# Kernel optimization log

Measured on AMD Instinct MI355X. Metric: run time of the kernel, lower is better.

## Reference

```python
import jax, jax.numpy as jnp
import numpy as np

NUM_NODES = 40000
NUM_REL = 474
ENT_DIM = 100
REL_DIM = 100
NHID = 100
NHEADS = 2
OUT_DIM = NHID * NHEADS  # 200
ALPHA = 0.2
NUM_ORTHO_HEADS = 2
ORTHO_LAMBDA = 0.01
EPS = 1e-12


def _l2norm(x):
    n = jnp.sqrt(jnp.sum(x * x, axis=1, keepdims=True))
    return x / jnp.maximum(n, EPS)


def _leaky_relu(x):
    return jnp.where(x >= 0, x, ALPHA * x)


def _ortho_loss(a):
    # orthogonality penalty between the NUM_ORTHO_HEADS row-blocks of `a`
    Af = a.reshape(NUM_ORTHO_HEADS, -1)
    Afn = Af / jnp.maximum(jnp.linalg.norm(Af, axis=1, keepdims=True), EPS)
    G = Afn @ Afn.T
    return ORTHO_LAMBDA * jnp.sum((G - jnp.eye(NUM_ORTHO_HEADS, dtype=a.dtype)) ** 2)


def _gat_layer(x, tgt, src, rel, a, a2, concat):
    # x: [N, f]; tgt/src: [E]; rel: [E, r]; a: [out, 2f+r]; a2: [out]
    f = x.shape[1]
    a_t, a_s, a_r = a[:, :f], a[:, f:2 * f], a[:, 2 * f:]
    # edge_m = a @ concat(x[tgt], x[src], rel)^T, computed without materializing the concat
    edge_m = x[tgt] @ a_t.T + x[src] @ a_s.T + rel @ a_r.T  # [E, out]
    powers = -_leaky_relu(edge_m @ a2)  # [E]
    edge_e = jnp.exp(powers)
    rowsum = jax.ops.segment_sum(edge_e, tgt, num_segments=NUM_NODES)  # [N]
    rowsum = jnp.where(rowsum == 0.0, EPS, rowsum)
    h = jax.ops.segment_sum(edge_e[:, None] * edge_m, tgt, num_segments=NUM_NODES)  # [N, out]
    h = h / rowsum[:, None]
    if concat:
        h = jax.nn.elu(h)
    return h, _ortho_loss(a)


def setup_inputs() -> dict:
    key = jax.random.key(0)
    ks = jax.random.split(key, 12)
    E, EN, B = 100000, 30000, 8192
    edge_list = jax.random.randint(ks[0], (2, E), 0, NUM_NODES)
    edge_type = jax.random.randint(ks[1], (E,), 0, NUM_REL)
    batch_inputs = jax.random.randint(ks[2], (B, 3), 0, NUM_REL)  # col 2 < 474 < NUM_NODES, valid node ids
    train_indices_nhop = jax.random.randint(ks[3], (EN, 4), 0, NUM_REL)
    s = 0.1
    entity_embeddings = jax.random.normal(ks[4], (NUM_NODES, ENT_DIM), jnp.float32)
    relation_embeddings = jax.random.normal(ks[5], (NUM_REL, REL_DIM), jnp.float32)
    W_entities = jax.random.normal(ks[6], (ENT_DIM, OUT_DIM), jnp.float32) * s
    W_rel = jax.random.normal(ks[7], (REL_DIM, OUT_DIM), jnp.float32) * s
    att_a = jax.random.normal(ks[8], (NHEADS, NHID, 2 * ENT_DIM + REL_DIM), jnp.float32) * s
    att_a2 = jax.random.normal(ks[9], (NHEADS, NHID), jnp.float32) * s
    out_a = jax.random.normal(ks[10], (OUT_DIM, 3 * OUT_DIM), jnp.float32) * s
    out_a2 = jax.random.normal(ks[11], (OUT_DIM,), jnp.float32) * s
    return {
        'edge_list': edge_list, 'edge_type': edge_type,
        'batch_inputs': batch_inputs, 'train_indices_nhop': train_indices_nhop,
        'entity_embeddings': entity_embeddings, 'relation_embeddings': relation_embeddings,
        'W_entities': W_entities, 'W_rel': W_rel,
        'att_a': att_a, 'att_a2': att_a2, 'out_a': out_a, 'out_a2': out_a2,
    }


def reference(edge_list, edge_type, batch_inputs, train_indices_nhop,
              entity_embeddings, relation_embeddings, W_entities, W_rel,
              att_a, att_a2, out_a, out_a2):
    ent = _l2norm(entity_embeddings)
    # edge lists: aggregation index is edge[0] (target); nhop edges = (col3, col0)
    tgt = jnp.concatenate([edge_list[0], train_indices_nhop[:, 3]])
    src = jnp.concatenate([edge_list[1], train_indices_nhop[:, 0]])
    # layer-1 relation features (1-hop gather + 2-hop sum fusion)
    rel1 = jnp.concatenate([
        relation_embeddings[edge_type],
        relation_embeddings[train_indices_nhop[:, 1]] + relation_embeddings[train_indices_nhop[:, 2]],
    ], axis=0)
    outs = []
    total_ortho = jnp.zeros((), dtype=ent.dtype)
    for i in range(NHEADS):
        h, ol = _gat_layer(ent, tgt, src, rel1, att_a[i], att_a2[i], True)
        outs.append(h)
        total_ortho = total_ortho + ol
    x = jnp.concatenate(outs, axis=1)  # [N, OUT_DIM]  (dropout skipped: eval mode)
    out_relation_1 = relation_embeddings @ W_rel  # [R, OUT_DIM]
    rel2 = jnp.concatenate([
        out_relation_1[edge_type],
        out_relation_1[train_indices_nhop[:, 1]] + out_relation_1[train_indices_nhop[:, 2]],
    ], axis=0)
    x, ol = _gat_layer(x, tgt, src, rel2, out_a, out_a2, False)
    total_ortho = total_ortho + ol
    mask = jnp.zeros((NUM_NODES,), dtype=x.dtype).at[batch_inputs[:, 2]].set(1.0)
    out_entity = ent @ W_entities + mask[:, None] * x
    out_entity = _l2norm(out_entity)
    return out_entity, out_relation_1, total_ortho
```

## Files before the change

### kernel.cpp

```cpp
#include <hip/hip_runtime.h>
#include <cstdint>
#include <cstddef>
#include <math.h>

#define N_NODES 40000
#define N_RELS  474
#define E0      100000
#define NE      130000
#define NB      8192
#define LRALPHA 0.2f

#define KP1 128
#define KP2 256
#define LD1 608
#define LD2 416
#define NPAD1 640
#define NPAD2 448
#define DTH 16
#define HUBW 2048

#define A_HIST   508
#define A_RELP   (A_HIST + 119)
#define A_MMW    (A_RELP + 32)
#define A_PACK1  (A_MMW + 320)
#define A_PACK2  (A_PACK1 + 448)
#define A_MASK   (A_PACK2 + 32)
#define A_TOT    (A_MASK + 128)
#define B_DR1    120
#define B_TOT    (B_DR1 + 32)
#define C_SCAT   508
#define C_GEMM   (C_SCAT + 1250)
#define C_CMP    (C_GEMM + 157)
#define C_DOTV   (C_CMP + 119)
#define C_TOT    (C_DOTV + 1)
#define N1_MAIN  2500
#define N1_HUB   (N1_MAIN + 512)
#define N1_TOT   (N1_HUB + 1250)

typedef __attribute__((ext_vector_type(8))) short short8;
typedef __attribute__((ext_vector_type(4))) float floatx4;

static __device__ __forceinline__ unsigned short f2bf(float f) {
    union { float f; uint32_t u; } v; v.f = f;
    uint32_t r = v.u + 0x7fff + ((v.u >> 16) & 1);
    return (unsigned short)(r >> 16);
}
static __device__ __forceinline__ float bf2f(unsigned short h) {
    union { uint32_t u; float f; } v; v.u = ((uint32_t)h) << 16;
    return v.f;
}
static __device__ __forceinline__ float bflo(uint32_t u) { return bf2f((unsigned short)(u & 0xffff)); }
static __device__ __forceinline__ float bfhi(uint32_t u) { return bf2f((unsigned short)(u >> 16)); }

static __device__ __forceinline__ int rdl(int v, int l) {
    return __builtin_amdgcn_readlane(v, l);
}
static __device__ __forceinline__ float rdlf(float v, int l) {
    return __int_as_float(__builtin_amdgcn_readlane(__float_as_int(v), l));
}
static __device__ __forceinline__ float frcp(float x) { return __builtin_amdgcn_rcpf(x); }


static __device__ void d_hist(int bid, int tid, const int* __restrict__ tgt_el,
                              const int* __restrict__ nhop, int* __restrict__ deg) {
    int e = bid * 256 + tid;
    if (e >= NE) return;
    int t = (e < E0) ? tgt_el[e] : nhop[(size_t)(e - E0) * 4 + 3];
    atomicAdd(&deg[t], 1);
}

static __device__ void d_mask(int bid, int tid, const int* __restrict__ batch,
                              float* __restrict__ mask) {
    int i = bid * 256 + tid;
    if (i < NB) mask[batch[(size_t)i * 3 + 2]] = 1.0f;
}

static __device__ void d_ortho_part(int bid, int tid, const float* __restrict__ att_a,
                                    const float* __restrict__ out_a, float* __restrict__ accum) {
    float loc[9] = {0,0,0,0,0,0,0,0,0};
    for (int i = bid * 256 + tid; i < 90000; i += 128 * 256) {
        int seg, li;
        const float* base;
        int L;
        if (i < 15000)      { seg = 0; li = i;          base = att_a;         L = 15000; }
        else if (i < 30000) { seg = 1; li = i - 15000;  base = att_a + 30000; L = 15000; }
        else                { seg = 2; li = i - 30000;  base = out_a;         L = 60000; }
        float a = base[li], b = base[L + li];
        loc[seg * 3 + 0] += a * a;
        loc[seg * 3 + 1] += b * b;
        loc[seg * 3 + 2] += a * b;
    }
    int lane = tid & 63;
#pragma unroll
    for (int q = 0; q < 9; q++) {
        float s = loc[q];
#pragma unroll
        for (int o = 32; o > 0; o >>= 1) s += __shfl_down(s, o);
        if (lane == 0 && s != 0.f) atomicAdd(&accum[q], s);
    }
}

static __device__ void d_scan2(int tid, int* wtot, int* __restrict__ bsums, int nb) {
    int v = (tid < nb) ? bsums[tid] : 0;
    int lane = tid & 63, wv = tid >> 6;
    int x = v;
#pragma unroll
    for (int o = 1; o < 64; o <<= 1) {
        int t = __shfl_up(x, o);
        if (lane >= o) x += t;
    }
    if (lane == 63) wtot[wv] = x;
    __syncthreads();
    int add = 0;
    for (int k = 0; k < wv; k++) add += wtot[k];
    __syncthreads();
    if (tid < nb) bsums[tid] = add + x - v;
    if (tid == 255) bsums[nb] = add + x;
}

static __device__ void d_pack1(int bid, int tid, const float* __restrict__ att_a,
                               const float* __restrict__ att_a2,
                               const float* __restrict__ W_ent,
                               unsigned short* __restrict__ W) {
    int idx = bid * 256 + tid;
    if (idx >= NPAD1 * KP1) return;
    int j = idx & 7;
    int lane = (idx >> 3) & 63;
    int u = idx >> 9;
    int ks = u & 3;
    int t = u >> 2;
    int r = t * 16 + (lane & 15);
    int k = ks * 32 + (lane >> 4) * 8 + j;
    float val = 0.f;
    if (k < 100) {
        if (r < 200) {
            int i = r >> 1, h = r & 1;
            val = att_a[h * 30000 + i * 300 + k];
        } else if (r < 400) {
            int rr = r - 200, i = rr >> 1, h = rr & 1;
            val = att_a[h * 30000 + i * 300 + 100 + k];
        } else if (r < 600) {
            val = W_ent[k * 200 + (r - 400)];
        } else if (r < 604) {
            int v = r - 600, head = v >> 1, part = v & 1;
            const float* base = att_a + head * 30000 + part * 100 + k;
            const float* a2v = att_a2 + head * 100;
            float s = 0.f;
            for (int n = 0; n < 100; n++) s += a2v[n] * base[n * 300];
            val = s;
        }
    }
    W[idx] = f2bf(val);
}

static __device__ void d_pack2(int bid, int tid, const float* __restrict__ out_a,
                               const float* __restrict__ out_a2,
                               unsigned short* __restrict__ W) {
    int idx = bid * 256 + tid;
    if (idx >= NPAD2 * KP2) return;
    int j = idx & 7;
    int lane = (idx >> 3) & 63;
    int u = idx >> 9;
    int ks = u & 7;
    int t = u >> 3;
    int r = t * 16 + (lane & 15);
    int k = ks * 32 + (lane >> 4) * 8 + j;
    float val = 0.f;
    if (k < 200) {
        int klog = (k & 1) * 100 + (k >> 1);
        if (r < 200)       val = out_a[r * 600 + klog];
        else if (r < 400)  val = out_a[(r - 200) * 600 + 200 + klog];
        else if (r == 400) {
            float s = 0.f;
            for (int n = 0; n < 200; n++) s += out_a2[n] * out_a[n * 600 + klog];
            val = s;
        } else if (r == 401) {
            float s = 0.f;
            for (int n = 0; n < 200; n++) s += out_a2[n] * out_a[n * 600 + 200 + klog];
            val = s;
        }
    }
    W[idx] = f2bf(val);
}

static __device__ void d_scatter(int bid, int tid, const int* __restrict__ tgt_el,
                                 const int* __restrict__ src_el, const int* __restrict__ etype,
                                 const int* __restrict__ nhop, int* __restrict__ cursor,
                                 int* __restrict__ srcs, int2* __restrict__ relpk) {
    int e = bid * 256 + tid;
    if (e >= NE) return;
    int t, s, r1, r2;
    if (e < E0) {
        t = tgt_el[e]; s = src_el[e]; r1 = etype[e]; r2 = -1;
    } else {
        const int* nh = nhop + (size_t)(e - E0) * 4;
        t = nh[3]; s = nh[0]; r1 = nh[1]; r2 = nh[2];
    }
    int p = atomicAdd(&cursor[t], 1);
    srcs[p] = s;
    relpk[p] = make_int2(r1, r2);
}

static __device__ void d_compact(int bid, int tid, const int* __restrict__ rowptr,
                                 const float* __restrict__ mask,
                                 int* __restrict__ Hlist, int* __restrict__ Mlist,
                                 int* __restrict__ cnts) {
    int i = bid * 256 + tid;
    if (i >= N_NODES) return;
    int deg = rowptr[i + 1] - rowptr[i];
    if (deg > DTH) { int p = atomicAdd(&cnts[0], 1); Hlist[p] = i; }
    if (mask[i] != 0.f) { int p = atomicAdd(&cnts[1], 1); Mlist[p] = i; }
}

template <int KP>
static __device__ void d_gemm(int bx, int by, char* smem_raw, int tid,
                              const unsigned short* __restrict__ A,
                              const unsigned short* __restrict__ B,
                              unsigned short* __restrict__ C,
                              int ldc, int N, int gPerSplit) {
    constexpr int KSTEPS = KP / 32;
    constexpr int KCH = KSTEPS / 4;
    unsigned short (*cbuf)[16][64] = (unsigned short (*)[16][64])smem_raw;
    int wave = tid >> 6;
    int lane = tid & 63;
    int quad = lane >> 4;
    int l16 = lane & 15;
    int m0 = bx * 64 + wave * 16;
    short8 afrag[KSTEPS];
    const unsigned short* arow = A + (size_t)(m0 + l16) * KP + quad * 8;
#pragma unroll
    for (int ks = 0; ks < KSTEPS; ks++)
        afrag[ks] = *(const short8*)(arow + ks * 32);

    int Gtot = (N + 63) >> 6;
    int g0 = by * gPerSplit;
    int g1 = g0 + gPerSplit;
    if (g1 > Gtot) g1 = Gtot;
    for (int g = g0; g < g1; g++) {
        int nb = g << 6;
        const unsigned short* bgrp = B + (((size_t)(g << 2) * KSTEPS) << 9) + (lane << 3);
        floatx4 acc[4];
#pragma unroll
        for (int t = 0; t < 4; t++) acc[t] = (floatx4){0.f, 0.f, 0.f, 0.f};
#pragma unroll
        for (int ch = 0; ch < KCH; ch++) {
            short8 bf[4][4];
#pragma unroll
            for (int t = 0; t < 4; t++)
#pragma unroll
                for (int k = 0; k < 4; k++)
                    bf[t][k] = *(const short8*)(bgrp + ((size_t)(t * KSTEPS + ch * 4 + k) << 9));
#pragma unroll
            for (int k = 0; k < 4; k++)
#pragma unroll
                for (int t = 0; t < 4; t++)
                    acc[t] = __builtin_amdgcn_mfma_f32_16x16x32_bf16(afrag[ch * 4 + k], bf[t][k], acc[t], 0, 0, 0);
        }
        int r0 = quad * 4;
#pragma unroll
        for (int t = 0; t < 4; t++)
#pragma unroll
            for (int i = 0; i < 4; i++)
                cbuf[wave][r0 + i][t * 16 + l16] = f2bf(acc[t][i]);
        int colsA = N - nb; if (colsA > 64) colsA = 64;
        int cols8 = colsA >> 3;
        int sh = (colsA >= 64) ? 3 : 2;
        int nchunks = cols8 << 4;
        for (int c = lane; c < nchunks; c += 64) {
            int row = c >> sh;
            int col8 = (c & (cols8 - 1)) << 3;
            *(uint4*)(C + (size_t)(m0 + row) * ldc + nb + col8) =
                *(const uint4*)&cbuf[wave][row][col8];
        }
    }
}

static __device__ void d_gemm1f(int bx, int by, char* smem_raw, int tid,
                                const float* __restrict__ ent,
                                const unsigned short* __restrict__ B,
                                unsigned short* __restrict__ C) {
    float (*rows)[105] = (float (*)[105])smem_raw;
    float* invn = (float*)(smem_raw + 64 * 105 * 4);
    int m0 = bx * 64;
    for (int idx = tid; idx < 6400; idx += 256) {
        int r = idx / 100, c = idx - r * 100;
        rows[r][c] = ent[(size_t)(m0 + r) * 100 + c];
    }
    __syncthreads();
    {
        int r = tid >> 2, q = tid & 3;
        const float* rp = rows[r] + q * 25;
        float s = 0.f;
#pragma unroll
        for (int c = 0; c < 25; c++) { float v = rp[c]; s += v * v; }
        s += __shfl_xor(s, 1);
        s += __shfl_xor(s, 2);
        if (q == 0) invn[r] = 1.f / fmaxf(sqrtf(s), 1e-12f);
    }
    __syncthreads();
    int wave = tid >> 6;
    int lane = tid & 63;
    int quad = lane >> 4;
    int l16 = lane & 15;
    int rr = wave * 16 + l16;
    float inv = invn[rr];
    short8 afrag[4];
#pragma unroll
    for (int ks = 0; ks < 4; ks++) {
        short8 f;
#pragma unroll
        for (int j = 0; j < 8; j++) {
            int col = ks * 32 + quad * 8 + j;
            f[j] = (col < 100) ? (short)f2bf(rows[rr][col] * inv) : (short)0;
        }
        afrag[ks] = f;
    }
    __syncthreads();
    unsigned short (*cbuf)[16][64] = (unsigned short (*)[16][64])smem_raw;
    int mo0 = m0 + wave * 16;
    int g0 = by * 5, g1 = g0 + 5;
    if (g1 > 10) g1 = 10;
    for (int g = g0; g < g1; g++) {
        int nb = g << 6;
        const unsigned short* bgrp = B + (((size_t)(g << 2) * 4) << 9) + (lane << 3);
        floatx4 acc[4];
#pragma unroll
        for (int t = 0; t < 4; t++) acc[t] = (floatx4){0.f, 0.f, 0.f, 0.f};
        short8 bf[4][4];
#pragma unroll
        for (int t = 0; t < 4; t++)
#pragma unroll
            for (int k = 0; k < 4; k++)
                bf[t][k] = *(const short8*)(bgrp + ((size_t)(t * 4 + k) << 9));
#pragma unroll
        for (int k = 0; k < 4; k++)
#pragma unroll
            for (int t = 0; t < 4; t++)
                acc[t] = __builtin_amdgcn_mfma_f32_16x16x32_bf16(afrag[k], bf[t][k], acc[t], 0, 0, 0);
        int r0 = quad * 4;
#pragma unroll
        for (int t = 0; t < 4; t++)
#pragma unroll
            for (int i = 0; i < 4; i++)
                cbuf[wave][r0 + i][t * 16 + l16] = f2bf(acc[t][i]);
        int colsA = 608 - nb; if (colsA > 64) colsA = 64;
        int cols8 = colsA >> 3;
        int sh = (colsA >= 64) ? 3 : 2;
        int nchunks = cols8 << 4;
        for (int c = lane; c < nchunks; c += 64) {
            int row = c >> sh;
            int col8 = (c & (cols8 - 1)) << 3;
            *(uint4*)(C + (size_t)(mo0 + row) * LD1 + nb + col8) =
                *(const uint4*)&cbuf[wave][row][col8];
        }
    }
}

template <bool BT>
static __device__ void d_mm(int bx, int by, char* smem_raw, int tid,
                            const float* __restrict__ A, int lda,
                            const float* __restrict__ B, int ldb,
                            float* __restrict__ C, int ldc,
                            int M, int N, int K) {
    float (*As)[65] = (float (*)[65])smem_raw;
    float (*Bs)[65] = (float (*)[65])(smem_raw + 16 * 65 * 4);
    int tx = tid & 15, ty = tid >> 4;
    int m0 = by * 64, n0 = bx * 64;
    float acc[4][4] = {};
    for (int k0 = 0; k0 < K; k0 += 16) {
        {
            int r = tid >> 2;
            int c4 = (tid & 3) * 4;
            int m = m0 + r;
#pragma unroll
            for (int u = 0; u < 4; u++) {
                int k = k0 + c4 + u;
                As[c4 + u][r] = (m < M && k < K) ? A[(size_t)m * lda + k] : 0.f;
            }
        }
        if (BT) {
            int r = tid >> 2;
            int c4 = (tid & 3) * 4;
            int n = n0 + r;
#pragma unroll
            for (int u = 0; u < 4; u++) {
                int k = k0 + c4 + u;
                Bs[c4 + u][r] = (n < N && k < K) ? B[(size_t)n * ldb + k] : 0.f;
            }
        } else {
            int kk = tid >> 4;
            int nn4 = (tid & 15) * 4;
            int k = k0 + kk;
#pragma unroll
            for (int u = 0; u < 4; u++) {
                int n = n0 + nn4 + u;
                Bs[kk][nn4 + u] = (k < K && n < N) ? B[(size_t)k * ldb + n] : 0.f;
            }
        }
        __syncthreads();
#pragma unroll
        for (int k = 0; k < 16; k++) {
            float a[4], b[4];
#pragma unroll
            for (int i = 0; i < 4; i++) a[i] = As[k][ty + 16 * i];
#pragma unroll
            for (int j = 0; j < 4; j++) b[j] = Bs[k][tx + 16 * j];
#pragma unroll
            for (int i = 0; i < 4; i++)
#pragma unroll
                for (int j = 0; j < 4; j++) acc[i][j] += a[i] * b[j];
        }
        __syncthreads();
    }
#pragma unroll
    for (int i = 0; i < 4; i++) {
        int m = m0 + ty + 16 * i;
        if (m >= M) continue;
#pragma unroll
        for (int j = 0; j < 4; j++) {
            int n = n0 + tx + 16 * j;
            if (n < N) C[(size_t)m * ldc + n] = acc[i][j];
        }
    }
}

static __device__ void d_relproj1(int bid, int tid, const float* __restrict__ rel_emb,
                                  const float* __restrict__ att_a, float* __restrict__ R1i) {
    int w = (bid * 256 + tid) >> 6;
    int lane = tid & 63;
    if (w >= N_RELS) return;
    const float* re = rel_emb + (size_t)w * 100;
    float2* dst = (float2*)(R1i + (size_t)w * 200);
    for (int f = lane; f < 100; f += 64) {
        const float* a0 = att_a + f * 300 + 200;
        const float* a1 = att_a + 30000 + f * 300 + 200;
        float s0 = 0.f, s1 = 0.f;
        for (int k = 0; k < 100; k++) {
            float rk = re[k];
            s0 += rk * a0[k];
            s1 += rk * a1[k];
        }
        dst[f] = make_float2(s0, s1);
    }
}

static __device__ void d_dR1(int bid, int tid, const float* __restrict__ R1i,
                             const float* __restrict__ att_a2,
                             float* __restrict__ dR10, float* __restrict__ dR11) {
    int w = (bid * 256 + tid) >> 6;
    int lane = tid & 63;
    if (w >= N_RELS) return;
    const float2* row = (const float2*)(R1i + (size_t)w * 200);
    float s0 = 0.f, s1 = 0.f;
    for (int f = lane; f < 100; f += 64) {
        float2 v = row[f];
        s0 += v.x * att_a2[f];
        s1 += v.y * att_a2[100 + f];
    }
#pragma unroll
    for (int o = 32; o > 0; o >>= 1) {
        s0 += __shfl_down(s0, o);
        s1 += __shfl_down(s1, o);
    }
    if (lane == 0) { dR10[w] = s0; dR11[w] = s1; }
}

static __device__ void d_ortho_fin(int tid, const float* __restrict__ accum,
                                   float* __restrict__ out_scalar) {
    if (tid != 0) return;
    float total = 0.f;
#pragma unroll
    for (int m = 0; m < 3; m++) {
        float s0 = accum[m * 3 + 0], s1 = accum[m * 3 + 1], sc = accum[m * 3 + 2];
        float c = sc / (fmaxf(sqrtf(s0), 1e-12f) * fmaxf(sqrtf(s1), 1e-12f));
        total += 0.01f * 2.f * c * c;
    }
    out_scalar[0] = total;
}


static __device__ void d_node1_one(int node, int lane,
                        const int* __restrict__ rowptr, const int* __restrict__ srcs,
                        const int2* __restrict__ relpk,
                        const unsigned short* __restrict__ Pcat,
                        const float* __restrict__ R1i,
                        const float* __restrict__ dR10, const float* __restrict__ dR11,
                        unsigned short* __restrict__ x) {
    bool fv = (lane < 50);
    int c4 = lane * 4;
    int beg = rowptr[node], end = rowptr[node + 1];
    int deg = end - beg;
    int fast = (deg < 64) ? deg : 64;
    uint2 td = *(const uint2*)(Pcat + (size_t)node * LD1 + 600);
    float t0h = bflo(td.x), t1h = bflo(td.y);
    int sL = 0, rxL = 0, ryL = -1;
    float wxL = 0.f, wyL = 0.f;
    if (lane < fast) {
        int p = beg + lane;
        sL = srcs[p];
        int2 rp = relpk[p];
        rxL = rp.x; ryL = rp.y;
        float dr0 = dR10[rp.x], dr1 = dR11[rp.x];
        if (rp.y >= 0) { dr0 += dR10[rp.y]; dr1 += dR11[rp.y]; }
        uint2 sd = *(const uint2*)(Pcat + (size_t)sL * LD1 + 600);
        float p0 = t0h + bfhi(sd.x) + dr0;
        float p1 = t1h + bfhi(sd.y) + dr1;
// ... 178 lines not shown
                v0 = (v0 > 0.f) ? v0 : __expf(v0) - 1.f;
                v1 = (v1 > 0.f) ? v1 : __expf(v1) - 1.f;
                v2 = (v2 > 0.f) ? v2 : __expf(v2) - 1.f;
                v3 = (v3 > 0.f) ? v3 : __expf(v3) - 1.f;
                uint2 w;
                w.x = (uint32_t)f2bf(v0) | ((uint32_t)f2bf(v1) << 16);
                w.y = (uint32_t)f2bf(v2) | ((uint32_t)f2bf(v3) << 16);
                *(uint2*)(xr + c4) = w;
            }
        } else {
            *(uint2*)(xr + 200 + (lane - 50) * 4) = make_uint2(0u, 0u);
        }
    }
}


static __device__ void d_node2_one(int node, int lane,
                        const int* __restrict__ rowptr, const int* __restrict__ srcs,
                        const int2* __restrict__ relpk,
                        const unsigned short* __restrict__ Qcat,
                        const unsigned short* __restrict__ Pcat,
                        const float* __restrict__ R2, const float* __restrict__ dR2,
                        const float* __restrict__ mask, float* __restrict__ out) {
    bool fv = (lane < 50);
    int c4 = lane * 4;
    int beg = rowptr[node], end = rowptr[node + 1];
    int deg = end - beg;
    int fast = (deg < 64) ? deg : 64;
    uint32_t tq = *(const uint32_t*)(Qcat + (size_t)node * LD2 + 400);
    float tdot = bflo(tq);
    int sL = 0, rxL = 0, ryL = -1;
    float WL = 0.f;
    if (lane < fast) {
        int p = beg + lane;
        sL = srcs[p];
        int2 rp = relpk[p];
        rxL = rp.x; ryL = rp.y;
        float dr = dR2[rp.x];
        if (rp.y >= 0) dr += dR2[rp.y];
        uint32_t sq = *(const uint32_t*)(Qcat + (size_t)sL * LD2 + 400);
        float pp = tdot + bfhi(sq) + dr;
        pp = (pp >= 0.f) ? pp : LRALPHA * pp;
        WL = __expf(-pp);
    }
    float c0 = 0.f, c1 = 0.f, c2 = 0.f, c3 = 0.f;
    float rs = 0.f;
    for (int j = 0; j < fast; j += 4) {
#pragma unroll
        for (int u = 0; u < 4; u++) {
            int jj = j + u;
            bool act = (jj < fast);
            int ls = act ? jj : 0;
            int sE = rdl(sL, ls);
            int rxE = rdl(rxL, ls);
            int ryE = act ? rdl(ryL, ls) : -1;
            float WE = act ? rdlf(WL, ls) : 0.f;
            uint2 qv = make_uint2(0u, 0u);
            float4 rv = make_float4(0.f, 0.f, 0.f, 0.f);
            if (fv) {
                qv = *(const uint2*)(Qcat + (size_t)sE * LD2 + 200 + c4);
                rv = *(const float4*)(R2 + (size_t)rxE * 200 + c4);
                if (ryE >= 0) {
                    float4 rb = *(const float4*)(R2 + (size_t)ryE * 200 + c4);
                    rv.x += rb.x; rv.y += rb.y; rv.z += rb.z; rv.w += rb.w;
                }
            }
            rs += WE;
            c0 += WE * (bflo(qv.x) + rv.x);
            c1 += WE * (bfhi(qv.x) + rv.y);
            c2 += WE * (bflo(qv.y) + rv.z);
            c3 += WE * (bfhi(qv.y) + rv.w);
        }
    }
    for (int p = beg + 64; p < end; p++) {
        int sE = srcs[p];
        int2 rp = relpk[p];
        float dr = dR2[rp.x];
        if (rp.y >= 0) dr += dR2[rp.y];
        uint32_t sq = *(const uint32_t*)(Qcat + (size_t)sE * LD2 + 400);
        float pp = tdot + bfhi(sq) + dr;
        pp = (pp >= 0.f) ? pp : LRALPHA * pp;
        float W = __expf(-pp);
        uint2 qv = make_uint2(0u, 0u);
        float4 rv = make_float4(0.f, 0.f, 0.f, 0.f);
        if (fv) {
            qv = *(const uint2*)(Qcat + (size_t)sE * LD2 + 200 + c4);
            rv = *(const float4*)(R2 + (size_t)rp.x * 200 + c4);
            if (rp.y >= 0) {
                float4 rb = *(const float4*)(R2 + (size_t)rp.y * 200 + c4);
                rv.x += rb.x; rv.y += rb.y; rv.z += rb.z; rv.w += rb.w;
            }
        }
        rs += W;
        c0 += W * (bflo(qv.x) + rv.x);
        c1 += W * (bfhi(qv.x) + rv.y);
        c2 += W * (bflo(qv.y) + rv.z);
        c3 += W * (bfhi(qv.y) + rv.w);
    }
    float d = (rs == 0.f) ? 1e-12f : rs;
    float idn = frcp(d);
    float mk = mask[node];
    float val0 = 0.f, val1 = 0.f, val2 = 0.f, val3 = 0.f;
    if (fv) {
        uint2 t = *(const uint2*)(Qcat + (size_t)node * LD2 + c4);
        uint2 e = *(const uint2*)(Pcat + (size_t)node * LD1 + 400 + c4);
        val0 = bflo(e.x) + mk * ((c0 + rs * bflo(t.x)) * idn);
        val1 = bfhi(e.x) + mk * ((c1 + rs * bfhi(t.x)) * idn);
        val2 = bflo(e.y) + mk * ((c2 + rs * bflo(t.y)) * idn);
        val3 = bfhi(e.y) + mk * ((c3 + rs * bfhi(t.y)) * idn);
    }
    float ss = val0 * val0 + val1 * val1 + val2 * val2 + val3 * val3;
#pragma unroll
    for (int o = 32; o > 0; o >>= 1) ss += __shfl_down(ss, o);
    ss = __shfl(ss, 0);
    float inv = frcp(fmaxf(sqrtf(ss), 1e-12f));
    if (fv) {
        *(float4*)(out + (size_t)node * 200 + c4) =
            make_float4(val0 * inv, val1 * inv, val2 * inv, val3 * inv);
    }
}


__global__ __launch_bounds__(256) void k_megaA(
        const int* __restrict__ tgt_el, const int* __restrict__ nhop, int* __restrict__ deg,
        const float* __restrict__ rel_emb, const float* __restrict__ att_a,
        float* __restrict__ R1i,
        const float* __restrict__ W_rel, float* __restrict__ outrel,
        const float* __restrict__ att_a2, const float* __restrict__ W_ent,
        unsigned short* __restrict__ W1,
        const float* __restrict__ out_a, const float* __restrict__ out_a2,
        unsigned short* __restrict__ W2,
        const int* __restrict__ batch, float* __restrict__ mask, float* __restrict__ oacc) {
    __shared__ __align__(16) char smem[8448];
    int bid = blockIdx.x, tid = threadIdx.x;
    if (bid < A_HIST) {
        d_hist(bid, tid, tgt_el, nhop, deg);
    } else if (bid < A_RELP) {
        d_relproj1(bid - A_HIST, tid, rel_emb, att_a, R1i);
    } else if (bid < A_MMW) {
        int i = bid - A_RELP;
        d_mm<false>(i & 3, i >> 2, smem, tid, rel_emb, 100, W_rel, 200, outrel, 200,
                    N_RELS, 200, 100);
    } else if (bid < A_PACK1) {
        d_pack1(bid - A_MMW, tid, att_a, att_a2, W_ent, W1);
    } else if (bid < A_PACK2) {
        d_pack2(bid - A_PACK1, tid, out_a, out_a2, W2);
    } else if (bid < A_MASK) {
        d_mask(bid - A_PACK2, tid, batch, mask);
    } else {
        d_ortho_part(bid - A_MASK, tid, att_a, out_a, oacc);
    }
}

__global__ void k_scan1(const int* __restrict__ deg, int* __restrict__ local,
                        int* __restrict__ bsums, int n) {
    int i = blockIdx.x * 256 + threadIdx.x;
    int v = (i < n) ? deg[i] : 0;
    int lane = threadIdx.x & 63;
    int wv = threadIdx.x >> 6;
    int x = v;
#pragma unroll
    for (int o = 1; o < 64; o <<= 1) {
        int t = __shfl_up(x, o);
        if (lane >= o) x += t;
    }
    __shared__ int wtot[4];
    if (lane == 63) wtot[wv] = x;
    __syncthreads();
    int add = 0;
    for (int k = 0; k < wv; k++) add += wtot[k];
    if (i < n) local[i] = add + x - v;
    if (threadIdx.x == 255) bsums[blockIdx.x] = add + x;
}

__global__ __launch_bounds__(256) void k_megaB(
        int* __restrict__ bsums, int nbk,
        const float* __restrict__ R1i, const float* __restrict__ att_a2,
        float* __restrict__ dR10, float* __restrict__ dR11,
        const float* __restrict__ outrel, const float* __restrict__ out_a,
        float* __restrict__ R2) {
    __shared__ __align__(16) char smem[8448];
    __shared__ int wtot[4];
    int bid = blockIdx.x, tid = threadIdx.x;
    if (bid == 0) {
        d_scan2(tid, wtot, bsums, nbk);
    } else if (bid < B_DR1) {
        d_dR1(bid - 1, tid, R1i, att_a2, dR10, dR11);
    } else {
        int i = bid - B_DR1;
        d_mm<true>(i & 3, i >> 2, smem, tid, outrel, 200, out_a + 400, 600, R2, 200,
                   N_RELS, 200, 200);
    }
}

__global__ void k_scan3(const int* __restrict__ local, const int* __restrict__ bsums,
                        int* __restrict__ rowptr, int* __restrict__ cursor, int n, int nb) {
    int i = blockIdx.x * 256 + threadIdx.x;
    if (i < n) {
        int v = local[i] + bsums[blockIdx.x];
        rowptr[i] = v;
        cursor[i] = v;
    } else if (i == n) {
        rowptr[n] = bsums[nb];
    }
}

__global__ __launch_bounds__(256) void k_megaC(
        const int* __restrict__ tgt_el, const int* __restrict__ src_el,
        const int* __restrict__ etype, const int* __restrict__ nhop, int* __restrict__ cursor,
        int* __restrict__ srcs, int2* __restrict__ relpk,
        const float* __restrict__ ent_emb, const unsigned short* __restrict__ Wcat1,
        unsigned short* __restrict__ Pcat,
        const int* __restrict__ rowptr, const float* __restrict__ mask,
        int* __restrict__ Hlist, int* __restrict__ Mlist, int* __restrict__ cnts,
        const float* __restrict__ R2, const float* __restrict__ out_a2,
        float* __restrict__ dR2,
        const float* __restrict__ oacc, float* __restrict__ oscalar) {
    __shared__ __align__(16) char smem[27392];
    int bid = blockIdx.x, tid = threadIdx.x;
    if (bid < C_SCAT) {
        d_scatter(bid, tid, tgt_el, src_el, etype, nhop, cursor, srcs, relpk);
    } else if (bid < C_GEMM) {
        int i = bid - C_SCAT;
        d_gemm1f(i % 625, i / 625, smem, tid, ent_emb, Wcat1, Pcat);
    } else if (bid < C_CMP) {
        d_compact(bid - C_GEMM, tid, rowptr, mask, Hlist, Mlist, cnts);
    } else if (bid < C_DOTV) {
        int w = (bid - C_CMP) * 4 + (tid >> 6);
        int lane = tid & 63;
        if (w < N_RELS) {
            const float* r = R2 + (size_t)w * 200;
            float s = 0.f;
            for (int j = lane; j < 200; j += 64) s += r[j] * out_a2[j];
#pragma unroll
            for (int o = 32; o > 0; o >>= 1) s += __shfl_down(s, o);
            if (lane == 0) dR2[w] = s;
        }
    } else {
        d_ortho_fin(tid, oacc, oscalar);
    }
}

__global__ __launch_bounds__(256, 4) void k_node1(
                        const int* __restrict__ rowptr, const int* __restrict__ srcs,
                        const int2* __restrict__ relpk,
                        const unsigned short* __restrict__ Pcat,
                        const float* __restrict__ R1i,
                        const float* __restrict__ dR10, const float* __restrict__ dR11,
                        unsigned short* __restrict__ x,
                        const int* __restrict__ Hlist, const int* __restrict__ cnts,
                        const float* __restrict__ mask, float* __restrict__ out) {
    int bid = blockIdx.x, tid = threadIdx.x;
    int lane = tid & 63;
    if (bid < N1_MAIN) {
        int wid = __builtin_amdgcn_readfirstlane(bid * 4 + (tid >> 6));
        d_node1_main(wid, lane, rowptr, srcs, relpk, Pcat, R1i, dR10, dR11, x);
    } else if (bid < N1_HUB) {
        int hw = (bid - N1_MAIN) * 4 + (tid >> 6);
        int cnt = cnts[0];
        for (int j = hw; j < cnt; j += HUBW) {
            int node = __builtin_amdgcn_readfirstlane(Hlist[j]);
            d_node1_one(node, lane, rowptr, srcs, relpk, Pcat, R1i, dR10, dR11, x);
        }
    } else {
        int wid = __builtin_amdgcn_readfirstlane((bid - N1_HUB) * 4 + (tid >> 6));
        int n0 = wid * 8;
        bool fv = (lane < 50);
        int c4 = lane * 4;
        float mval = (lane < 8) ? mask[n0 + lane] : 0.f;
        uint2 e[8];
#pragma unroll
        for (int i = 0; i < 8; i++)
            e[i] = fv ? *(const uint2*)(Pcat + (size_t)(n0 + i) * LD1 + 400 + c4)
                      : make_uint2(0u, 0u);
#pragma unroll
        for (int i = 0; i < 8; i++) {
            if (rdlf(mval, i) != 0.f) continue;
            float v0 = bflo(e[i].x), v1 = bfhi(e[i].x);
            float v2 = bflo(e[i].y), v3 = bfhi(e[i].y);
            float ss = v0 * v0 + v1 * v1 + v2 * v2 + v3 * v3;
#pragma unroll
            for (int o = 32; o > 0; o >>= 1) ss += __shfl_down(ss, o);
            ss = __shfl(ss, 0);
            float inv = frcp(fmaxf(sqrtf(ss), 1e-12f));
            if (fv) {
                *(float4*)(out + (size_t)(n0 + i) * 200 + c4) =
                    make_float4(v0 * inv, v1 * inv, v2 * inv, v3 * inv);
            }
        }
    }
}

__global__ __launch_bounds__(256) void k_gemm2(const unsigned short* __restrict__ A,
                                               const unsigned short* __restrict__ B,
                                               unsigned short* __restrict__ C,
                                               int ldc, int N, int gPerSplit) {
    __shared__ __align__(16) char smem[8192];
    d_gemm<KP2>(blockIdx.x, blockIdx.y, smem, threadIdx.x, A, B, C, ldc, N, gPerSplit);
}

__global__ __launch_bounds__(256, 4) void k_node2h(
                        const int* __restrict__ rowptr, const int* __restrict__ srcs,
                        const int2* __restrict__ relpk,
                        const unsigned short* __restrict__ Qcat,
                        const unsigned short* __restrict__ Pcat,
                        const float* __restrict__ R2, const float* __restrict__ dR2,
                        const float* __restrict__ mask,
                        const int* __restrict__ Mlist, const int* __restrict__ cnts,
                        float* __restrict__ out) {
    int tid = threadIdx.x;
    int lane = tid & 63;
    int hw = blockIdx.x * 4 + (tid >> 6);
    int cnt = cnts[1];
    for (int j = hw; j < cnt; j += HUBW) {
        int node = __builtin_amdgcn_readfirstlane(Mlist[j]);
        d_node2_one(node, lane, rowptr, srcs, relpk, Qcat, Pcat, R2, dR2, mask, out);
    }
}

extern "C" void kernel_launch(void* const* d_in, const int* in_sizes, int n_in,
                              void* d_out, int out_size, void* d_ws, size_t ws_size,
                              hipStream_t stream) {
    const int* edge_list = (const int*)d_in[0];
    const int* edge_type = (const int*)d_in[1];
    const int* batch     = (const int*)d_in[2];
    const int* nhop      = (const int*)d_in[3];
    const float* ent_emb = (const float*)d_in[4];
    const float* rel_emb = (const float*)d_in[5];
    const float* W_ent   = (const float*)d_in[6];
    const float* W_rel   = (const float*)d_in[7];
    const float* att_a   = (const float*)d_in[8];
    const float* att_a2  = (const float*)d_in[9];
    const float* out_a   = (const float*)d_in[10];
    const float* out_a2  = (const float*)d_in[11];
    float* out = (float*)d_out;
    const int* tgt_el = edge_list;
    const int* src_el = edge_list + E0;

    char* ws = (char*)d_ws;
    size_t o = 0;
    auto alloc = [&](size_t nbytes) -> char* {
        char* p = ws + o;
        o += (nbytes + 255) & ~(size_t)255;
        return p;
    };
    unsigned short* x_bf    = (unsigned short*)alloc((size_t)N_NODES * KP2 * 2);
    unsigned short* Pcat    = (unsigned short*)alloc((size_t)N_NODES * LD1 * 2);
    unsigned short* Qcat    = (unsigned short*)alloc((size_t)N_NODES * LD2 * 2);
    unsigned short* Wcat1   = (unsigned short*)alloc((size_t)NPAD1 * KP1 * 2);
    unsigned short* Wcat2   = (unsigned short*)alloc((size_t)NPAD2 * KP2 * 2);
    float* R1i   = (float*)alloc(474u * 200 * 4);
    float* R2    = (float*)alloc(474u * 200 * 4);
    float* dR10  = (float*)alloc(474u * 4);
    float* dR11  = (float*)alloc(474u * 4);
    float* dR2   = (float*)alloc(474u * 4);
    int* rowptr  = (int*)alloc((N_NODES + 1) * 4);
    int* cursor  = (int*)alloc(N_NODES * 4);
    int* srcs    = (int*)alloc((size_t)NE * 4);
    int2* relpk  = (int2*)alloc((size_t)NE * 8);
    float* mask  = (float*)alloc(N_NODES * 4);
    int* scanloc = (int*)alloc(N_NODES * 4);
    int* bsums   = (int*)alloc(260 * 4);
    float* oacc  = (float*)alloc(9 * 4);
    int* Hlist   = (int*)alloc(N_NODES * 4);
    int* Mlist   = (int*)alloc(N_NODES * 4);
    int* cnts    = (int*)alloc(2 * 4);

    hipMemsetAsync(cursor, 0, N_NODES * 4, stream);
    hipMemsetAsync(mask, 0, N_NODES * 4, stream);
    hipMemsetAsync(oacc, 0, 9 * 4, stream);
    hipMemsetAsync(cnts, 0, 2 * 4, stream);

    k_megaA<<<A_TOT, 256, 0, stream>>>(tgt_el, nhop, cursor,
                                       rel_emb, att_a, R1i,
                                       W_rel, out + 8000000,
                                       att_a2, W_ent, Wcat1,
                                       out_a, out_a2, Wcat2,
                                       batch, mask, oacc);
    k_scan1<<<157, 256, 0, stream>>>(cursor, scanloc, bsums, N_NODES);
    k_megaB<<<B_TOT, 256, 0, stream>>>(bsums, 157, R1i, att_a2, dR10, dR11,
                                       out + 8000000, out_a, R2);
    k_scan3<<<157, 256, 0, stream>>>(scanloc, bsums, rowptr, cursor, N_NODES, 157);
    k_megaC<<<C_TOT, 256, 0, stream>>>(tgt_el, src_el, edge_type, nhop, cursor,
                                       srcs, relpk, ent_emb, Wcat1, Pcat,
                                       rowptr, mask, Hlist, Mlist, cnts,
                                       R2, out_a2, dR2, oacc, out + 8094800);
    k_node1<<<N1_TOT, 256, 0, stream>>>(rowptr, srcs, relpk, Pcat, R1i, dR10, dR11,
                                        x_bf, Hlist, cnts, mask, out);
    k_gemm2<<<dim3(625, 2), 256, 0, stream>>>(x_bf, Wcat2, Qcat, LD2, 416, 4);
    k_node2h<<<512, 256, 0, stream>>>(rowptr, srcs, relpk, Qcat, Pcat, R2, dR2,
                                      mask, Mlist, cnts, out);
}
```

Baseline: 326.9 us.

## Merge three-pass degree scan into one block and fuse unmasked row normalisation into GEMM

Replaces the three-kernel prefix scan (block scan, block-sum scan, add-back) with a single-block full scan over all 40000 degrees inside the existing B kernel, removing two launches. Also moves the l2-normalised output for unmasked nodes out of k_node1 and into the layer-1 GEMM epilogue, using the entity-projection columns already held in shared memory instead of rereading them from Pcat. The single-block scan serialises about 40 iterations on one workgroup, which may lengthen the B kernel's critical path, and the GEMM blocks gain extra shared memory and epilogue work.

```diff
diff --git a/kernel.cpp b/kernel.cpp
--- a/kernel.cpp
+++ b/kernel.cpp
@@ -34,8 +34,7 @@
 #define C_DOTV   (C_CMP + 119)
 #define C_TOT    (C_DOTV + 1)
 #define N1_MAIN  2500
-#define N1_HUB   (N1_MAIN + 512)
-#define N1_TOT   (N1_HUB + 1250)
+#define N1_TOT   (N1_MAIN + 512)
 
 typedef __attribute__((ext_vector_type(8))) short short8;
 typedef __attribute__((ext_vector_type(4))) float floatx4;
@@ -100,22 +99,37 @@
     }
 }
 
-static __device__ void d_scan2(int tid, int* wtot, int* __restrict__ bsums, int nb) {
-    int v = (tid < nb) ? bsums[tid] : 0;
+static __device__ void d_fullscan(int tid, int* degcur, int* rowptr) {
+    __shared__ int wsum[4];
     int lane = tid & 63, wv = tid >> 6;
-    int x = v;
-#pragma unroll
-    for (int o = 1; o < 64; o <<= 1) {
-        int t = __shfl_up(x, o);
-        if (lane >= o) x += t;
-    }
-    if (lane == 63) wtot[wv] = x;
-    __syncthreads();
-    int add = 0;
-    for (int k = 0; k < wv; k++) add += wtot[k];
-    __syncthreads();
-    if (tid < nb) bsums[tid] = add + x - v;
-    if (tid == 255) bsums[nb] = add + x;
+    int carry = 0;
+    for (int base = 0; base < N_NODES; base += 1024) {
+        int i0 = base + tid * 4;
+        int v0 = (i0 + 0 < N_NODES) ? degcur[i0 + 0] : 0;
+        int v1 = (i0 + 1 < N_NODES) ? degcur[i0 + 1] : 0;
+        int v2 = (i0 + 2 < N_NODES) ? degcur[i0 + 2] : 0;
+        int v3 = (i0 + 3 < N_NODES) ? degcur[i0 + 3] : 0;
+        int s1 = v0 + v1, s2 = s1 + v2, tot = s2 + v3;
+        int x = tot;
+#pragma unroll
+        for (int o = 1; o < 64; o <<= 1) {
+            int t = __shfl_up(x, o);
+            if (lane >= o) x += t;
+        }
+        if (lane == 63) wsum[wv] = x;
+        __syncthreads();
+        int add = carry;
+        for (int k = 0; k < wv; k++) add += wsum[k];
+        int excl = add + x - tot;
+        if (i0 + 0 < N_NODES) { rowptr[i0 + 0] = excl;      degcur[i0 + 0] = excl; }
+        if (i0 + 1 < N_NODES) { rowptr[i0 + 1] = excl + v0; degcur[i0 + 1] = excl + v0; }
+        if (i0 + 2 < N_NODES) { rowptr[i0 + 2] = excl + s1; degcur[i0 + 2] = excl + s1; }
+        if (i0 + 3 < N_NODES) { rowptr[i0 + 3] = excl + s2; degcur[i0 + 3] = excl + s2; }
+        int tot_all = wsum[0] + wsum[1] + wsum[2] + wsum[3];
+        __syncthreads();
+        carry += tot_all;
+    }
+    if (tid == 0) rowptr[N_NODES] = carry;
 }
 
 static __device__ void d_pack1(int bid, int tid, const float* __restrict__ att_a,
@@ -278,9 +292,12 @@
 static __device__ void d_gemm1f(int bx, int by, char* smem_raw, int tid,
                                 const float* __restrict__ ent,
                                 const unsigned short* __restrict__ B,
-                                unsigned short* __restrict__ C) {
+                                unsigned short* __restrict__ C,
+                                const float* __restrict__ mask,
+                                float* __restrict__ out) {
     float (*rows)[105] = (float (*)[105])smem_raw;
     float* invn = (float*)(smem_raw + 64 * 105 * 4);
+    unsigned short (*entw)[200] = (unsigned short (*)[200])(smem_raw + 8192);
     int m0 = bx * 64;
     for (int idx = tid; idx < 6400; idx += 256) {
         int r = idx / 100, c = idx - r * 100;
@@ -352,6 +369,40 @@
             int col8 = (c & (cols8 - 1)) << 3;
             *(uint4*)(C + (size_t)(mo0 + row) * LD1 + nb + col8) =
                 *(const uint4*)&cbuf[wave][row][col8];
+        }
+        if (by == 1) {
+            int cg = nb + lane;
+            if (cg >= 400 && cg < 600) {
+#pragma unroll
+                for (int i = 0; i < 16; i++)
+                    entw[wave * 16 + i][cg - 400] = cbuf[wave][i][lane];
+            }
+        }
+    }
+    if (by == 1) {
+        bool fv = (lane < 50);
+        int c4 = lane * 4;
+        for (int i = 0; i < 16; i++) {
+            int row = wave * 16 + i;
+            int node = m0 + row;
+            float mk = mask[node];
+            if (mk != 0.f) continue;
+            float v0 = 0.f, v1 = 0.f, v2 = 0.f, v3 = 0.f;
+            if (fv) {
+                v0 = bf2f(entw[row][c4 + 0]);
+                v1 = bf2f(entw[row][c4 + 1]);
+                v2 = bf2f(entw[row][c4 + 2]);
+                v3 = bf2f(entw[row][c4 + 3]);
+            }
+            float ss = v0 * v0 + v1 * v1 + v2 * v2 + v3 * v3;
+#pragma unroll
+            for (int o = 32; o > 0; o >>= 1) ss += __shfl_down(ss, o);
+            ss = __shfl(ss, 0);
+            float iv = frcp(fmaxf(sqrtf(ss), 1e-12f));
+            if (fv) {
+                *(float4*)(out + (size_t)node * 200 + c4) =
+                    make_float4(v0 * iv, v1 * iv, v2 * iv, v3 * iv);
+            }
         }
     }
 }
@@ -836,56 +887,22 @@
     }
 }
 
-__global__ void k_scan1(const int* __restrict__ deg, int* __restrict__ local,
-                        int* __restrict__ bsums, int n) {
-    int i = blockIdx.x * 256 + threadIdx.x;
-    int v = (i < n) ? deg[i] : 0;
-    int lane = threadIdx.x & 63;
-    int wv = threadIdx.x >> 6;
-    int x = v;
-#pragma unroll
-    for (int o = 1; o < 64; o <<= 1) {
-        int t = __shfl_up(x, o);
-        if (lane >= o) x += t;
-    }
-    __shared__ int wtot[4];
-    if (lane == 63) wtot[wv] = x;
-    __syncthreads();
-    int add = 0;
-    for (int k = 0; k < wv; k++) add += wtot[k];
-    if (i < n) local[i] = add + x - v;
-    if (threadIdx.x == 255) bsums[blockIdx.x] = add + x;
-}
-
-__global__ __launch_bounds__(256) void k_megaB(
-        int* __restrict__ bsums, int nbk,
+__global__ __launch_bounds__(256) void k_scanB(
+        int* __restrict__ degcur, int* __restrict__ rowptr,
         const float* __restrict__ R1i, const float* __restrict__ att_a2,
         float* __restrict__ dR10, float* __restrict__ dR11,
         const float* __restrict__ outrel, const float* __restrict__ out_a,
         float* __restrict__ R2) {
     __shared__ __align__(16) char smem[8448];
-    __shared__ int wtot[4];
     int bid = blockIdx.x, tid = threadIdx.x;
     if (bid == 0) {
-        d_scan2(tid, wtot, bsums, nbk);
+        d_fullscan(tid, degcur, rowptr);
     } else if (bid < B_DR1) {
         d_dR1(bid - 1, tid, R1i, att_a2, dR10, dR11);
     } else {
         int i = bid - B_DR1;
         d_mm<true>(i & 3, i >> 2, smem, tid, outrel, 200, out_a + 400, 600, R2, 200,
                    N_RELS, 200, 200);
-    }
-}
-
-__global__ void k_scan3(const int* __restrict__ local, const int* __restrict__ bsums,
-                        int* __restrict__ rowptr, int* __restrict__ cursor, int n, int nb) {
-    int i = blockIdx.x * 256 + threadIdx.x;
-    if (i < n) {
-        int v = local[i] + bsums[blockIdx.x];
-        rowptr[i] = v;
-        cursor[i] = v;
-    } else if (i == n) {
-        rowptr[n] = bsums[nb];
     }
 }
 
@@ -899,14 +916,15 @@
         int* __restrict__ Hlist, int* __restrict__ Mlist, int* __restrict__ cnts,
         const float* __restrict__ R2, const float* __restrict__ out_a2,
         float* __restrict__ dR2,
-        const float* __restrict__ oacc, float* __restrict__ oscalar) {
-    __shared__ __align__(16) char smem[27392];
+        const float* __restrict__ oacc, float* __restrict__ oscalar,
+        float* __restrict__ outbuf) {
+    __shared__ __align__(16) char smem[33792];
     int bid = blockIdx.x, tid = threadIdx.x;
     if (bid < C_SCAT) {
         d_scatter(bid, tid, tgt_el, src_el, etype, nhop, cursor, srcs, relpk);
     } else if (bid < C_GEMM) {
         int i = bid - C_SCAT;
-        d_gemm1f(i % 625, i / 625, smem, tid, ent_emb, Wcat1, Pcat);
+        d_gemm1f(i % 625, i / 625, smem, tid, ent_emb, Wcat1, Pcat, mask, outbuf);
     } else if (bid < C_CMP) {
         d_compact(bid - C_GEMM, tid, rowptr, mask, Hlist, Mlist, cnts);
     } else if (bid < C_DOTV) {
@@ -932,45 +950,18 @@
                         const float* __restrict__ R1i,
                         const float* __restrict__ dR10, const float* __restrict__ dR11,
                         unsigned short* __restrict__ x,
-                        const int* __restrict__ Hlist, const int* __restrict__ cnts,
-                        const float* __restrict__ mask, float* __restrict__ out) {
+                        const int* __restrict__ Hlist, const int* __restrict__ cnts) {
     int bid = blockIdx.x, tid = threadIdx.x;
     int lane = tid & 63;
     if (bid < N1_MAIN) {
         int wid = __builtin_amdgcn_readfirstlane(bid * 4 + (tid >> 6));
         d_node1_main(wid, lane, rowptr, srcs, relpk, Pcat, R1i, dR10, dR11, x);
-    } else if (bid < N1_HUB) {
+    } else {
         int hw = (bid - N1_MAIN) * 4 + (tid >> 6);
         int cnt = cnts[0];
         for (int j = hw; j < cnt; j += HUBW) {
             int node = __builtin_amdgcn_readfirstlane(Hlist[j]);
             d_node1_one(node, lane, rowptr, srcs, relpk, Pcat, R1i, dR10, dR11, x);
-        }
-    } else {
-        int wid = __builtin_amdgcn_readfirstlane((bid - N1_HUB) * 4 + (tid >> 6));
-        int n0 = wid * 8;
-        bool fv = (lane < 50);
-        int c4 = lane * 4;
-        float mval = (lane < 8) ? mask[n0 + lane] : 0.f;
-        uint2 e[8];
-#pragma unroll
-        for (int i = 0; i < 8; i++)
-            e[i] = fv ? *(const uint2*)(Pcat + (size_t)(n0 + i) * LD1 + 400 + c4)
-                      : make_uint2(0u, 0u);
-#pragma unroll
-        for (int i = 0; i < 8; i++) {
-            if (rdlf(mval, i) != 0.f) continue;
-            float v0 = bflo(e[i].x), v1 = bfhi(e[i].x);
-            float v2 = bflo(e[i].y), v3 = bfhi(e[i].y);
-            float ss = v0 * v0 + v1 * v1 + v2 * v2 + v3 * v3;
-#pragma unroll
-            for (int o = 32; o > 0; o >>= 1) ss += __shfl_down(ss, o);
-            ss = __shfl(ss, 0);
-            float inv = frcp(fmaxf(sqrtf(ss), 1e-12f));
-            if (fv) {
-                *(float4*)(out + (size_t)(n0 + i) * 200 + c4) =
-                    make_float4(v0 * inv, v1 * inv, v2 * inv, v3 * inv);
-            }
         }
     }
 }
@@ -1043,8 +1034,6 @@
     int* srcs    = (int*)alloc((size_t)NE * 4);
     int2* relpk  = (int2*)alloc((size_t)NE * 8);
     float* mask  = (float*)alloc(N_NODES * 4);
-    int* scanloc = (int*)alloc(N_NODES * 4);
-    int* bsums   = (int*)alloc(260 * 4);
     float* oacc  = (float*)alloc(9 * 4);
     int* Hlist   = (int*)alloc(N_NODES * 4);
     int* Mlist   = (int*)alloc(N_NODES * 4);
@@ -1061,16 +1050,14 @@
                                        att_a2, W_ent, Wcat1,
                                        out_a, out_a2, Wcat2,
                                        batch, mask, oacc);
-    k_scan1<<<157, 256, 0, stream>>>(cursor, scanloc, bsums, N_NODES);
-    k_megaB<<<B_TOT, 256, 0, stream>>>(bsums, 157, R1i, att_a2, dR10, dR11,
+    k_scanB<<<B_TOT, 256, 0, stream>>>(cursor, rowptr, R1i, att_a2, dR10, dR11,
                                        out + 8000000, out_a, R2);
-    k_scan3<<<157, 256, 0, stream>>>(scanloc, bsums, rowptr, cursor, N_NODES, 157);
     k_megaC<<<C_TOT, 256, 0, stream>>>(tgt_el, src_el, edge_type, nhop, cursor,
                                        srcs, relpk, ent_emb, Wcat1, Pcat,
                                        rowptr, mask, Hlist, Mlist, cnts,
-                                       R2, out_a2, dR2, oacc, out + 8094800);
+                                       R2, out_a2, dR2, oacc, out + 8094800, out);
     k_node1<<<N1_TOT, 256, 0, stream>>>(rowptr, srcs, relpk, Pcat, R1i, dR10, dR11,
-                                        x_bf, Hlist, cnts, mask, out);
+                                        x_bf, Hlist, cnts);
     k_gemm2<<<dim3(625, 2), 256, 0, stream>>>(x_bf, Wcat2, Qcat, LD2, 416, 4);
     k_node2h<<<512, 256, 0, stream>>>(rowptr, srcs, relpk, Qcat, Pcat, R2, dR2,
                                       mask, Mlist, cnts, out);
```

Measured after the change: 346.3 us. 5.9% more time.

## Move layer-1 node GEMM into scan kernel and fuse unmasked-row L2 normalize

Applied to the files above, without the earlier changes.

Moves the fused entity GEMM (d_gemm1f) from megaC into megaB, so it runs alongside the prefix scan and dR1 blocks. The GEMM epilogue now also L2-normalizes and writes the output rows of unmasked nodes directly from shared memory, which removes a separate pass in k_node1 that reread Pcat. The dR2 dot-product blocks move into the scan3 kernel, leaving megaC with only scatter, compact and ortho-finalize. In exchange, megaB needs much more shared memory, which may reduce occupancy.

```diff
diff --git a/kernel.cpp b/kernel.cpp
--- a/kernel.cpp
+++ b/kernel.cpp
@@ -26,16 +26,17 @@
 #define A_PACK2  (A_PACK1 + 448)
 #define A_MASK   (A_PACK2 + 32)
 #define A_TOT    (A_MASK + 128)
-#define B_DR1    120
-#define B_TOT    (B_DR1 + 32)
-#define C_SCAT   508
-#define C_GEMM   (C_SCAT + 1250)
-#define C_CMP    (C_GEMM + 157)
-#define C_DOTV   (C_CMP + 119)
-#define C_TOT    (C_DOTV + 1)
+#define B_G1F    1
+#define B_DR1    (B_G1F + 1250)
+#define B_R2     (B_DR1 + 119)
+#define B_TOT    (B_R2 + 32)
+#define S3_DOTV  157
+#define S3_TOT   (S3_DOTV + 119)
+#define C_CMP    508
+#define C_OFIN   (C_CMP + 157)
+#define C_TOT    (C_OFIN + 1)
 #define N1_MAIN  2500
-#define N1_HUB   (N1_MAIN + 512)
-#define N1_TOT   (N1_HUB + 1250)
+#define N1_TOT   (N1_MAIN + 512)
 
 typedef __attribute__((ext_vector_type(8))) short short8;
 typedef __attribute__((ext_vector_type(4))) float floatx4;
@@ -278,9 +279,12 @@
 static __device__ void d_gemm1f(int bx, int by, char* smem_raw, int tid,
                                 const float* __restrict__ ent,
                                 const unsigned short* __restrict__ B,
-                                unsigned short* __restrict__ C) {
+                                unsigned short* __restrict__ C,
+                                const float* __restrict__ mask,
+                                float* __restrict__ out) {
     float (*rows)[105] = (float (*)[105])smem_raw;
     float* invn = (float*)(smem_raw + 64 * 105 * 4);
+    unsigned short (*entw)[200] = (unsigned short (*)[200])(smem_raw + 8192);
     int m0 = bx * 64;
     for (int idx = tid; idx < 6400; idx += 256) {
         int r = idx / 100, c = idx - r * 100;
@@ -352,6 +356,40 @@
             int col8 = (c & (cols8 - 1)) << 3;
             *(uint4*)(C + (size_t)(mo0 + row) * LD1 + nb + col8) =
                 *(const uint4*)&cbuf[wave][row][col8];
+        }
+        if (by == 1) {
+            int cg = nb + lane;
+            if (cg >= 400 && cg < 600) {
+#pragma unroll
+                for (int i = 0; i < 16; i++)
+                    entw[wave * 16 + i][cg - 400] = cbuf[wave][i][lane];
+            }
+        }
+    }
+    if (by == 1) {
+        bool fv = (lane < 50);
+        int c4 = lane * 4;
+        for (int i = 0; i < 16; i++) {
+            int row = wave * 16 + i;
+            int node = m0 + row;
+            float mk = mask[node];
+            if (mk != 0.f) continue;
+            float v0 = 0.f, v1 = 0.f, v2 = 0.f, v3 = 0.f;
+            if (fv) {
+                v0 = bf2f(entw[row][c4 + 0]);
+                v1 = bf2f(entw[row][c4 + 1]);
+                v2 = bf2f(entw[row][c4 + 2]);
+                v3 = bf2f(entw[row][c4 + 3]);
+            }
+            float ss = v0 * v0 + v1 * v1 + v2 * v2 + v3 * v3;
+#pragma unroll
+            for (int o = 32; o > 0; o >>= 1) ss += __shfl_down(ss, o);
+            ss = __shfl(ss, 0);
+            float iv = frcp(fmaxf(sqrtf(ss), 1e-12f));
+            if (fv) {
+                *(float4*)(out + (size_t)node * 200 + c4) =
+                    make_float4(v0 * iv, v1 * iv, v2 * iv, v3 * iv);
+            }
         }
     }
 }
@@ -859,58 +897,46 @@
 
 __global__ __launch_bounds__(256) void k_megaB(
         int* __restrict__ bsums, int nbk,
+        const float* __restrict__ ent_emb, const unsigned short* __restrict__ Wcat1,
+        unsigned short* __restrict__ Pcat,
+        const float* __restrict__ mask, float* __restrict__ outbuf,
         const float* __restrict__ R1i, const float* __restrict__ att_a2,
         float* __restrict__ dR10, float* __restrict__ dR11,
         const float* __restrict__ outrel, const float* __restrict__ out_a,
         float* __restrict__ R2) {
-    __shared__ __align__(16) char smem[8448];
+    __shared__ __align__(16) char smem[33792];
     __shared__ int wtot[4];
     int bid = blockIdx.x, tid = threadIdx.x;
     if (bid == 0) {
         d_scan2(tid, wtot, bsums, nbk);
     } else if (bid < B_DR1) {
-        d_dR1(bid - 1, tid, R1i, att_a2, dR10, dR11);
+        int i = bid - B_G1F;
+        d_gemm1f(i % 625, i / 625, smem, tid, ent_emb, Wcat1, Pcat, mask, outbuf);
+    } else if (bid < B_R2) {
+        d_dR1(bid - B_DR1, tid, R1i, att_a2, dR10, dR11);
     } else {
-        int i = bid - B_DR1;
+        int i = bid - B_R2;
         d_mm<true>(i & 3, i >> 2, smem, tid, outrel, 200, out_a + 400, 600, R2, 200,
                    N_RELS, 200, 200);
     }
 }
 
-__global__ void k_scan3(const int* __restrict__ local, const int* __restrict__ bsums,
-                        int* __restrict__ rowptr, int* __restrict__ cursor, int n, int nb) {
-    int i = blockIdx.x * 256 + threadIdx.x;
-    if (i < n) {
-        int v = local[i] + bsums[blockIdx.x];
-        rowptr[i] = v;
-        cursor[i] = v;
-    } else if (i == n) {
-        rowptr[n] = bsums[nb];
-    }
-}
-
-__global__ __launch_bounds__(256) void k_megaC(
-        const int* __restrict__ tgt_el, const int* __restrict__ src_el,
-        const int* __restrict__ etype, const int* __restrict__ nhop, int* __restrict__ cursor,
-        int* __restrict__ srcs, int2* __restrict__ relpk,
-        const float* __restrict__ ent_emb, const unsigned short* __restrict__ Wcat1,
-        unsigned short* __restrict__ Pcat,
-        const int* __restrict__ rowptr, const float* __restrict__ mask,
-        int* __restrict__ Hlist, int* __restrict__ Mlist, int* __restrict__ cnts,
-        const float* __restrict__ R2, const float* __restrict__ out_a2,
-        float* __restrict__ dR2,
-        const float* __restrict__ oacc, float* __restrict__ oscalar) {
-    __shared__ __align__(16) char smem[27392];
+__global__ void k_scan3d(const int* __restrict__ local, const int* __restrict__ bsums,
+                         int* __restrict__ rowptr, int* __restrict__ cursor, int n, int nb,
+                         const float* __restrict__ R2, const float* __restrict__ out_a2,
+                         float* __restrict__ dR2) {
     int bid = blockIdx.x, tid = threadIdx.x;
-    if (bid < C_SCAT) {
-        d_scatter(bid, tid, tgt_el, src_el, etype, nhop, cursor, srcs, relpk);
-    } else if (bid < C_GEMM) {
-        int i = bid - C_SCAT;
-        d_gemm1f(i % 625, i / 625, smem, tid, ent_emb, Wcat1, Pcat);
-    } else if (bid < C_CMP) {
-        d_compact(bid - C_GEMM, tid, rowptr, mask, Hlist, Mlist, cnts);
-    } else if (bid < C_DOTV) {
-        int w = (bid - C_CMP) * 4 + (tid >> 6);
+    if (bid < S3_DOTV) {
+        int i = bid * 256 + tid;
+        if (i < n) {
+            int v = local[i] + bsums[bid];
+            rowptr[i] = v;
+            cursor[i] = v;
+        } else if (i == n) {
+            rowptr[n] = bsums[nb];
+        }
+    } else {
+        int w = (bid - S3_DOTV) * 4 + (tid >> 6);
         int lane = tid & 63;
         if (w < N_RELS) {
             const float* r = R2 + (size_t)w * 200;
@@ -920,6 +946,21 @@
             for (int o = 32; o > 0; o >>= 1) s += __shfl_down(s, o);
             if (lane == 0) dR2[w] = s;
         }
+    }
+}
+
+__global__ __launch_bounds__(256) void k_megaC(
+        const int* __restrict__ tgt_el, const int* __restrict__ src_el,
+        const int* __restrict__ etype, const int* __restrict__ nhop, int* __restrict__ cursor,
+        int* __restrict__ srcs, int2* __restrict__ relpk,
+        const int* __restrict__ rowptr, const float* __restrict__ mask,
+        int* __restrict__ Hlist, int* __restrict__ Mlist, int* __restrict__ cnts,
+        const float* __restrict__ oacc, float* __restrict__ oscalar) {
+    int bid = blockIdx.x, tid = threadIdx.x;
+    if (bid < C_CMP) {
+        d_scatter(bid, tid, tgt_el, src_el, etype, nhop, cursor, srcs, relpk);
+    } else if (bid < C_OFIN) {
+        d_compact(bid - C_CMP, tid, rowptr, mask, Hlist, Mlist, cnts);
     } else {
         d_ortho_fin(tid, oacc, oscalar);
     }
@@ -932,45 +973,18 @@
                         const float* __restrict__ R1i,
                         const float* __restrict__ dR10, const float* __restrict__ dR11,
                         unsigned short* __restrict__ x,
-                        const int* __restrict__ Hlist, const int* __restrict__ cnts,
-                        const float* __restrict__ mask, float* __restrict__ out) {
+                        const int* __restrict__ Hlist, const int* __restrict__ cnts) {
     int bid = blockIdx.x, tid = threadIdx.x;
     int lane = tid & 63;
     if (bid < N1_MAIN) {
         int wid = __builtin_amdgcn_readfirstlane(bid * 4 + (tid >> 6));
         d_node1_main(wid, lane, rowptr, srcs, relpk, Pcat, R1i, dR10, dR11, x);
-    } else if (bid < N1_HUB) {
+    } else {
         int hw = (bid - N1_MAIN) * 4 + (tid >> 6);
         int cnt = cnts[0];
         for (int j = hw; j < cnt; j += HUBW) {
             int node = __builtin_amdgcn_readfirstlane(Hlist[j]);
             d_node1_one(node, lane, rowptr, srcs, relpk, Pcat, R1i, dR10, dR11, x);
-        }
-    } else {
-        int wid = __builtin_amdgcn_readfirstlane((bid - N1_HUB) * 4 + (tid >> 6));
-        int n0 = wid * 8;
-        bool fv = (lane < 50);
-        int c4 = lane * 4;
-        float mval = (lane < 8) ? mask[n0 + lane] : 0.f;
-        uint2 e[8];
-#pragma unroll
-        for (int i = 0; i < 8; i++)
-            e[i] = fv ? *(const uint2*)(Pcat + (size_t)(n0 + i) * LD1 + 400 + c4)
-                      : make_uint2(0u, 0u);
-#pragma unroll
-        for (int i = 0; i < 8; i++) {
-            if (rdlf(mval, i) != 0.f) continue;
-            float v0 = bflo(e[i].x), v1 = bfhi(e[i].x);
-            float v2 = bflo(e[i].y), v3 = bfhi(e[i].y);
-            float ss = v0 * v0 + v1 * v1 + v2 * v2 + v3 * v3;
-#pragma unroll
-            for (int o = 32; o > 0; o >>= 1) ss += __shfl_down(ss, o);
-            ss = __shfl(ss, 0);
-            float inv = frcp(fmaxf(sqrtf(ss), 1e-12f));
-            if (fv) {
-                *(float4*)(out + (size_t)(n0 + i) * 200 + c4) =
-                    make_float4(v0 * inv, v1 * inv, v2 * inv, v3 * inv);
-            }
         }
     }
 }
@@ -1062,15 +1076,16 @@
                                        out_a, out_a2, Wcat2,
                                        batch, mask, oacc);
     k_scan1<<<157, 256, 0, stream>>>(cursor, scanloc, bsums, N_NODES);
-    k_megaB<<<B_TOT, 256, 0, stream>>>(bsums, 157, R1i, att_a2, dR10, dR11,
+    k_megaB<<<B_TOT, 256, 0, stream>>>(bsums, 157, ent_emb, Wcat1, Pcat, mask, out,
+                                       R1i, att_a2, dR10, dR11,
                                        out + 8000000, out_a, R2);
-    k_scan3<<<157, 256, 0, stream>>>(scanloc, bsums, rowptr, cursor, N_NODES, 157);
+    k_scan3d<<<S3_TOT, 256, 0, stream>>>(scanloc, bsums, rowptr, cursor, N_NODES, 157,
+                                         R2, out_a2, dR2);
     k_megaC<<<C_TOT, 256, 0, stream>>>(tgt_el, src_el, edge_type, nhop, cursor,
-                                       srcs, relpk, ent_emb, Wcat1, Pcat,
-                                       rowptr, mask, Hlist, Mlist, cnts,
-                                       R2, out_a2, dR2, oacc, out + 8094800);
+                                       srcs, relpk, rowptr, mask, Hlist, Mlist, cnts,
+                                       oacc, out + 8094800);
     k_node1<<<N1_TOT, 256, 0, stream>>>(rowptr, srcs, relpk, Pcat, R1i, dR10, dR11,
-                                        x_bf, Hlist, cnts, mask, out);
+                                        x_bf, Hlist, cnts);
     k_gemm2<<<dim3(625, 2), 256, 0, stream>>>(x_bf, Wcat2, Qcat, LD2, 416, 4);
     k_node2h<<<512, 256, 0, stream>>>(rowptr, srcs, relpk, Qcat, Pcat, R2, dR2,
                                       mask, Mlist, cnts, out);
```

Measured after the change: 323.0 us. About the same (-1.2%).
